# Kernel tuning notes

Hardware: AMD Instinct MI355X
Metric: run time of the kernel (lower is better)

Reference implementation:

```python
import jax, jax.numpy as jnp
import numpy as np

B, DETER, STOCH, ACT_DIM, HIDDEN, BLOCKS, DEMB = 4096, 4096, 1024, 32, 512, 8, 16
EPS = 1e-4
OUT_B = DETER // BLOCKS            # 512 per-block output
IN_B0 = 4 * HIDDEN + OUT_B          # 2560 per-block input of first hidden block-GEMM


def rmsnorm(x, g):
    return x * jax.lax.rsqrt(jnp.mean(x * x, axis=-1, keepdims=True) + EPS) * g


def setup_inputs() -> dict:
    key = jax.random.key(0)
    ks = jax.random.split(key, 16)
    n = lambda k, s: (jax.random.normal(k, s, jnp.float32) * 0.02)
    return {
        'stoch': jax.random.normal(ks[0], (B, STOCH), jnp.float32),
        'deter': jax.random.normal(ks[1], (B, DETER), jnp.float32),
        'action': jax.random.normal(ks[2], (B, ACT_DIM), jnp.float32),
        'd_emb': jax.random.normal(ks[3], (B, DEMB), jnp.float32),
        # four input branches: Linear -> RMSNorm -> SiLU
        'W0': n(ks[4], (DETER, HIDDEN)), 'b0': jnp.zeros(HIDDEN), 'g0': jnp.ones(HIDDEN),
        'W1': n(ks[5], (STOCH, HIDDEN)), 'b1': jnp.zeros(HIDDEN), 'g1': jnp.ones(HIDDEN),
        'W2': n(ks[6], (ACT_DIM, HIDDEN)), 'b2': jnp.zeros(HIDDEN), 'g2': jnp.ones(HIDDEN),
        'W3': n(ks[7], (DEMB, HIDDEN)), 'b3': jnp.zeros(HIDDEN), 'g3': jnp.ones(HIDDEN),
        # block-diagonal hidden layers (dynlayers=2)
        'Wh0': n(ks[8], (BLOCKS, IN_B0, OUT_B)), 'bh0': jnp.zeros(DETER), 'gh0': jnp.ones(DETER),
        'Wh1': n(ks[9], (BLOCKS, OUT_B, OUT_B)), 'bh1': jnp.zeros(DETER), 'gh1': jnp.ones(DETER),
        # block-diagonal GRU gate projection: deter -> 3*deter
        'Wg': n(ks[10], (BLOCKS, OUT_B, 3 * OUT_B)), 'bg': jnp.zeros(3 * DETER),
    }


def reference(stoch, deter, action, d_emb,
              W0, b0, g0, W1, b1, g1, W2, b2, g2, W3, b3, g3,
              Wh0, bh0, gh0, Wh1, bh1, gh1, Wg, bg):
    act = jax.nn.silu
    Bsz = action.shape[0]
    stoch = stoch.reshape(Bsz, -1)
    # action / clip(|action|, min=1).detach()
    action = action / jax.lax.stop_gradient(jnp.maximum(jnp.abs(action), 1.0))

    x0 = act(rmsnorm(deter @ W0 + b0, g0))
    x1 = act(rmsnorm(stoch @ W1 + b1, g1))
    x2 = act(rmsnorm(action @ W2 + b2, g2))
    x3 = act(rmsnorm(d_emb @ W3 + b3, g3))
    x = jnp.concatenate([x0, x1, x2, x3], axis=-1)          # [B, 4H]

    xg = jnp.broadcast_to(x[:, None, :], (Bsz, BLOCKS, 4 * HIDDEN))
    dg = deter.reshape(Bsz, BLOCKS, OUT_B)                   # flat2group(deter)
    h = jnp.concatenate([dg, xg], axis=-1)                   # [B, blocks, in_b0]

    # hidden layer 0: BlockLinear -> RMSNorm(full width) -> act
    h = jnp.einsum('bgi,gio->bgo', h, Wh0).reshape(Bsz, DETER) + bh0
    h = act(rmsnorm(h, gh0))
    # hidden layer 1
    h = jnp.einsum('bgi,gio->bgo', h.reshape(Bsz, BLOCKS, OUT_B), Wh1).reshape(Bsz, DETER) + bh1
    h = act(rmsnorm(h, gh1))

    # GRU gates via block-diagonal GEMM: [B, blocks, 3*out_b]
    gates = jnp.einsum('bgi,gio->bgo', h.reshape(Bsz, BLOCKS, OUT_B), Wg).reshape(Bsz, 3 * DETER) + bg
    gg = gates.reshape(Bsz, BLOCKS, 3 * OUT_B)
    reset = gg[..., :OUT_B].reshape(Bsz, DETER)
    cand = gg[..., OUT_B:2 * OUT_B].reshape(Bsz, DETER)
    update = gg[..., 2 * OUT_B:].reshape(Bsz, DETER)

    reset = jax.nn.sigmoid(reset)
    cand = jnp.tanh(reset * cand)
    update = jax.nn.sigmoid(update - 1.0)
    return update * cand + (1.0 - update) * deter
```

## Files before the change

### kernel.cpp

```cpp
#include <hip/hip_runtime.h>
#include <hip/hip_bf16.h>
#include <cstdint>

typedef __bf16 bf16x8 __attribute__((ext_vector_type(8)));
typedef float f32x4 __attribute__((ext_vector_type(4)));
typedef unsigned short u16x8 __attribute__((ext_vector_type(8)));
typedef unsigned short u16x4 __attribute__((ext_vector_type(4)));

__device__ __forceinline__ unsigned short f2bf(float f) {
  unsigned int u = __float_as_uint(f);
  u += 0x7FFFu + ((u >> 16) & 1u);
  return (unsigned short)(u >> 16);
}
__device__ __forceinline__ float bf2f(unsigned short h) {
  return __uint_as_float(((unsigned int)h) << 16);
}
__device__ __forceinline__ float frcp_(float x) { return __builtin_amdgcn_rcpf(x); }
__device__ __forceinline__ float sigmoid_fast(float x) { return frcp_(1.f + __expf(-x)); }
__device__ __forceinline__ float tanh_fast(float x) { return 1.f - 2.f * frcp_(__expf(2.f * x) + 1.f); }
__device__ __forceinline__ float siluf_(float x) { return x * sigmoid_fast(x); }

#define GLOAD_LDS16(gsrc, ldst) \
  __builtin_amdgcn_global_load_lds((const __attribute__((address_space(1))) void*)(gsrc), \
                                   (__attribute__((address_space(3))) void*)(ldst), 16, 0, 0)

#define S_BARRIER() asm volatile("s_barrier" ::: "memory")
#define LGKM0() asm volatile("s_waitcnt lgkmcnt(0)" ::: "memory")

__device__ __forceinline__ void xcd_tile(int& x, int& y, int& z) {
  const int gx = gridDim.x, gy = gridDim.y;
  const int nwg = gx * gy * gridDim.z;
  const int lin = (blockIdx.z * gy + blockIdx.y) * gx + blockIdx.x;
  const int cpx = nwg >> 3;
  const int t = (lin & 7) * cpx + (lin >> 3);
  x = t % gx;
  const int r = t / gx;
  y = r % gy;
  z = r / gy;
}

template<int F32>
__device__ __forceinline__ void gemm8_core(
    const unsigned short* __restrict__ A1, int lda1, int K1,
    const unsigned short* __restrict__ A2, int lda2, int K2,
    const unsigned short* __restrict__ Bt, int ldb,
    void* __restrict__ C, int ldc,
    int tm, int tn, unsigned short* lds)
{
  const int tid = threadIdx.x;
  const int lane = tid & 63;
  const int wave = tid >> 6;
  const int wm = (wave >> 2) * 128;
  const int wn = (wave & 3) * 64;
  const int frow = lane & 15;
  const int chunk16 = (lane >> 4) * 16;
  const int nt = (K1 + K2) >> 5;
  const int S = nt >> 1;

  auto stageA = [&](unsigned short* dstA, int ktBase) {
    const unsigned short* Ab; int alda, kloc;
    if (ktBase >= K1) { Ab = A2; alda = lda2; kloc = ktBase - K1; }
    else              { Ab = A1; alda = lda1; kloc = ktBase; }
#pragma unroll
    for (int j = 0; j < 2; ++j) {
      int o = j * 8192 + tid * 16;
      int so = o ^ (((o >> 7) & 3) << 4);
      int row = so >> 6, cb = so & 63;
      GLOAD_LDS16(Ab + (long long)(tm + row) * alda + kloc + (cb >> 1),
                  (char*)dstA + j * 8192 + wave * 1024);
    }
  };
  auto stageB = [&](unsigned short* dstB, int ktBase) {
#pragma unroll
    for (int j = 0; j < 2; ++j) {
      int o = j * 8192 + tid * 16;
      int so = o ^ (((o >> 7) & 3) << 4);
      int row = so >> 6, cb = so & 63;
      GLOAD_LDS16(Bt + (long long)(tn + row) * ldb + ktBase + (cb >> 1),
                  (char*)dstB + j * 8192 + wave * 1024);
    }
  };
  auto ldswz = [&](const unsigned short* rg, int row) -> bf16x8 {
    int o = row * 64 + chunk16;
    o ^= ((o >> 7) & 3) << 4;
    return *(const bf16x8*)((const char*)rg + o);
  };

  f32x4 acc[8][4] = {};

  stageA(lds, 0);             stageB(lds + 8192, 0);
  stageA(lds + 16384, 32);    stageB(lds + 24576, 32);
  asm volatile("s_waitcnt vmcnt(0)" ::: "memory");
  S_BARRIER();

  for (int s = 0; s < S; ++s) {
    const int t = 2 * s;
    unsigned short* b0 = lds + (t & 3) * 16384;
    unsigned short* b1 = lds + ((t + 1) & 3) * 16384;
    if (s > 0) {
      LGKM0();
      S_BARRIER();
    }
    if (s + 1 < S) {
      unsigned short* s0 = lds + ((t + 2) & 3) * 16384;
      unsigned short* s1 = lds + ((t + 3) & 3) * 16384;
      stageA(s0, (t + 2) * 32); stageB(s0 + 8192, (t + 2) * 32);
      stageA(s1, (t + 3) * 32); stageB(s1 + 8192, (t + 3) * 32);
      asm volatile("s_waitcnt vmcnt(8)" ::: "memory");
    } else {
      asm volatile("s_waitcnt vmcnt(0)" ::: "memory");
    }
    S_BARRIER();
    {
      bf16x8 av[4], bv[4];
#pragma unroll
      for (int j = 0; j < 4; ++j) bv[j] = ldswz(b0 + 8192, wn + j * 16 + frow);
#pragma unroll
      for (int i = 0; i < 4; ++i) av[i] = ldswz(b0, wm + i * 16 + frow);
      __builtin_amdgcn_s_setprio(1);
#pragma unroll
      for (int i = 0; i < 4; ++i)
#pragma unroll
        for (int j = 0; j < 4; ++j)
          acc[i][j] = __builtin_amdgcn_mfma_f32_16x16x32_bf16(av[i], bv[j], acc[i][j], 0, 0, 0);
#pragma unroll
      for (int i = 0; i < 4; ++i) av[i] = ldswz(b0, wm + 64 + i * 16 + frow);
#pragma unroll
      for (int i = 0; i < 4; ++i)
#pragma unroll
        for (int j = 0; j < 4; ++j)
          acc[4 + i][j] = __builtin_amdgcn_mfma_f32_16x16x32_bf16(av[i], bv[j], acc[4 + i][j], 0, 0, 0);
      __builtin_amdgcn_s_setprio(0);
    }
    {
      bf16x8 av[4], bv[4];
#pragma unroll
      for (int j = 0; j < 4; ++j) bv[j] = ldswz(b1 + 8192, wn + j * 16 + frow);
#pragma unroll
      for (int i = 0; i < 4; ++i) av[i] = ldswz(b1, wm + i * 16 + frow);
      __builtin_amdgcn_s_setprio(1);
#pragma unroll
      for (int i = 0; i < 4; ++i)
#pragma unroll
        for (int j = 0; j < 4; ++j)
          acc[i][j] = __builtin_amdgcn_mfma_f32_16x16x32_bf16(av[i], bv[j], acc[i][j], 0, 0, 0);
#pragma unroll
      for (int i = 0; i < 4; ++i) av[i] = ldswz(b1, wm + 64 + i * 16 + frow);
#pragma unroll
      for (int i = 0; i < 4; ++i)
#pragma unroll
        for (int j = 0; j < 4; ++j)
          acc[4 + i][j] = __builtin_amdgcn_mfma_f32_16x16x32_bf16(av[i], bv[j], acc[4 + i][j], 0, 0, 0);
      __builtin_amdgcn_s_setprio(0);
    }
  }

  const int cr = (lane >> 4) * 4;
  const int cc = lane & 15;
#pragma unroll
  for (int mf = 0; mf < 8; ++mf) {
    const int r0 = tm + wm + mf * 16 + cr;
#pragma unroll
    for (int j = 0; j < 4; ++j) {
      const int col = tn + wn + j * 16 + cc;
#pragma unroll
      for (int i = 0; i < 4; ++i) {
        if (F32) ((float*)C)[(long long)(r0 + i) * ldc + col] = acc[mf][j][i];
        else ((unsigned short*)C)[(long long)(r0 + i) * ldc + col] = f2bf(acc[mf][j][i]);
      }
    }
  }
}

__global__ __launch_bounds__(512, 2) void gemm8(
    const unsigned short* __restrict__ A1, int lda1, long long a1_bs, int K1,
    const unsigned short* __restrict__ A2, int lda2, int K2,
    const unsigned short* __restrict__ Bt, int ldb, long long bt_bs,
    unsigned short* __restrict__ C, int ldc, long long c_bs)
{
  __shared__ unsigned short lds[4 * 16384];
  int tx, ty, g;
  xcd_tile(tx, ty, g);
  gemm8_core<0>(A1 + (long long)g * a1_bs, lda1, K1, A2, lda2, K2,
                Bt + (long long)g * bt_bs, ldb,
                C + (long long)g * c_bs, ldc,
                ty * 256, tx * 256, lds);
}

struct BCfg { const unsigned short* A; int lda; int K;
              const unsigned short* Bt; int ldb; float* C; };
struct BPack { BCfg c[9]; };
__global__ __launch_bounds__(512, 2) void gemm8_branch(BPack p) {
  __shared__ unsigned short lds[4 * 16384];
  int tx, ty, z;
  xcd_tile(tx, ty, z);
  BCfg c = p.c[z];
  gemm8_core<1>(c.A, c.lda, c.K, nullptr, 0, 0, c.Bt, c.ldb, c.C, 512,
                ty * 256, tx * 256, lds);
}

__global__ __launch_bounds__(512, 2) void gemm_gru(
    const unsigned short* __restrict__ hB,
    const unsigned short* __restrict__ Wgt,
    const float* __restrict__ bg,
    const unsigned short* __restrict__ deterB,
    float* __restrict__ out)
{
  __shared__ unsigned short lds[4 * 14336];
  int txi, tyi, g;
  xcd_tile(txi, tyi, g);
  const int tm = tyi * 256;
  const int tn = txi * 192;
  const unsigned short* A  = hB + g * 512;
  const unsigned short* Bt = Wgt + (long long)g * 1536 * 512;
  const int tid = threadIdx.x, lane = tid & 63, wave = tid >> 6;
  const int wm = (wave >> 2) * 128;
  const int wv = wave & 3;
  const int frow = lane & 15, chunk16 = (lane >> 4) * 16;
  const bool wlow = (wave < 4);
  const int S = 8;

  auto stageA = [&](unsigned short* buf, int kt) {
#pragma unroll
    for (int j = 0; j < 2; ++j) {
      int o = j * 8192 + tid * 16;
      int so = o ^ (((o >> 7) & 3) << 4);
      int row = so >> 6, cb = so & 63;
      GLOAD_LDS16(A + (long long)(tm + row) * 4096 + kt + (cb >> 1),
                  (char*)buf + j * 8192 + wave * 1024);
    }
  };
  auto stageB = [&](unsigned short* buf, int kt) {
    char* bb = (char*)(buf + 8192);
    {
      int o = tid * 16;
      int so = o ^ (((o >> 7) & 3) << 4);
      int row = so >> 6, cb = so & 63;
      GLOAD_LDS16(Bt + (long long)(tn + row) * 512 + kt + (cb >> 1),
                  bb + wave * 1024);
    }
    if (tid < 256) {
      int o = 8192 + tid * 16;
      int so = o ^ (((o >> 7) & 3) << 4);
      int row = so >> 6, cb = so & 63;
      GLOAD_LDS16(Bt + (long long)(tn + row) * 512 + kt + (cb >> 1),
                  bb + 8192 + wave * 1024);
    }
  };
  auto ldA = [&](const unsigned short* buf, int row) -> bf16x8 {
    int o = row * 64 + chunk16; o ^= ((o >> 7) & 3) << 4;
    return *(const bf16x8*)((const char*)buf + o);
  };
  auto ldB = [&](const unsigned short* buf, int nf) -> bf16x8 {
    int row = wv * 48 + nf * 16 + frow;
    int o = row * 64 + chunk16; o ^= ((o >> 7) & 3) << 4;
    return *(const bf16x8*)((const char*)(buf + 8192) + o);
  };

  f32x4 acc[8][3] = {};

  stageA(lds, 0);             stageB(lds, 0);
  stageA(lds + 14336, 32);    stageB(lds + 14336, 32);
  asm volatile("s_waitcnt vmcnt(0)" ::: "memory");
  S_BARRIER();

  for (int s = 0; s < S; ++s) {
    const int t = 2 * s;
    unsigned short* b0 = lds + (t & 3) * 14336;
    unsigned short* b1 = lds + ((t + 1) & 3) * 14336;
    if (s > 0) {
      LGKM0();
      S_BARRIER();
    }
    if (s + 1 < S) {
      unsigned short* s0 = lds + ((t + 2) & 3) * 14336;
      unsigned short* s1 = lds + ((t + 3) & 3) * 14336;
      stageA(s0, (t + 2) * 32); stageB(s0, (t + 2) * 32);
      stageA(s1, (t + 3) * 32); stageB(s1, (t + 3) * 32);
      if (wlow) asm volatile("s_waitcnt vmcnt(8)" ::: "memory");
      else      asm volatile("s_waitcnt vmcnt(6)" ::: "memory");
    } else {
      asm volatile("s_waitcnt vmcnt(0)" ::: "memory");
    }
    S_BARRIER();
#pragma unroll
    for (int half = 0; half < 2; ++half) {
      const unsigned short* bb = half ? b1 : b0;
      bf16x8 av[4], bv[3];
#pragma unroll
      for (int j = 0; j < 3; ++j) bv[j] = ldB(bb, j);
#pragma unroll
      for (int i = 0; i < 4; ++i) av[i] = ldA(bb, wm + i * 16 + frow);
      __builtin_amdgcn_s_setprio(1);
#pragma unroll
      for (int i = 0; i < 4; ++i)
#pragma unroll
        for (int j = 0; j < 3; ++j)
          acc[i][j] = __builtin_amdgcn_mfma_f32_16x16x32_bf16(av[i], bv[j], acc[i][j], 0, 0, 0);
#pragma unroll
      for (int i = 0; i < 4; ++i) av[i] = ldA(bb, wm + 64 + i * 16 + frow);
#pragma unroll
      for (int i = 0; i < 4; ++i)
#pragma unroll
        for (int j = 0; j < 3; ++j)
          acc[4 + i][j] = __builtin_amdgcn_mfma_f32_16x16x32_bf16(av[i], bv[j], acc[4 + i][j], 0, 0, 0);
      __builtin_amdgcn_s_setprio(0);
    }
  }

  const int cr = (lane >> 4) * 4, cc = lane & 15;
  const int o_col = (txi * 4 + wv) * 16 + cc;
  const int gcol = g * 512 + o_col;
  const float bgr = bg[g * 1536 + o_col];
  const float bgc = bg[g * 1536 + 512 + o_col];
  const float bgu = bg[g * 1536 + 1024 + o_col];
#pragma unroll
  for (int mf = 0; mf < 8; ++mf) {
    const int r0 = tm + wm + mf * 16 + cr;
#pragma unroll
    for (int i = 0; i < 4; ++i) {
      const long long off = (long long)(r0 + i) * 4096 + gcol;
      float dt = bf2f(deterB[off]);
      float reset = sigmoid_fast(acc[mf][0][i] + bgr);
      float cand  = tanh_fast(reset * (acc[mf][1][i] + bgc));
      float upd   = sigmoid_fast(acc[mf][2][i] + bgu - 1.f);
      out[off] = upd * cand + (1.f - upd) * dt;
    }
  }
}

__device__ __forceinline__ void transpose_dev(
    const float* __restrict__ src, unsigned short* __restrict__ dst,
    int R, int C, int bx, int by, int bz, float (*t)[132])
{
  const long long bOff = (long long)bz * R * C;
  src += bOff; dst += bOff;
  const int c0 = bx * 128, r0 = by * 32;
  const int tid = threadIdx.x;
  const int tx = tid & 31, ty = tid >> 5;
#pragma unroll
  for (int j = 0; j < 4; ++j) {
    int row = ty + j * 8;
    float4 v = *(const float4*)&src[(long long)(r0 + row) * C + c0 + tx * 4];
    *(float4*)&t[row][tx * 4] = v;
  }
  __syncthreads();
#pragma unroll
  for (int j = 0; j < 4; ++j) {
    int idx = j * 256 + tid;
    int c = idx >> 3, rg = idx & 7;
    u16x4 o;
    o.x = f2bf(t[rg * 4 + 0][c]); o.y = f2bf(t[rg * 4 + 1][c]);
    o.z = f2bf(t[rg * 4 + 2][c]); o.w = f2bf(t[rg * 4 + 3][c]);
    *(u16x4*)&dst[(long long)(c0 + c) * R + r0 + rg * 4] = o;
  }
}

__device__ __forceinline__ void transpose_wg_dev(
    const float* __restrict__ src, unsigned short* __restrict__ dst,
    int bx, int by, int bz, float (*t)[132])
{
  src += (long long)bz * 512 * 1536;
  dst += (long long)bz * 1536 * 512;
  const int c0 = bx * 128, r0 = by * 32;
  const int tid = threadIdx.x;
  const int tx = tid & 31, ty = tid >> 5;
#pragma unroll
  for (int j = 0; j < 4; ++j) {
    int row = ty + j * 8;
    float4 v = *(const float4*)&src[(long long)(r0 + row) * 1536 + c0 + tx * 4];
    *(float4*)&t[row][tx * 4] = v;
  }
  __syncthreads();
#pragma unroll
  for (int j = 0; j < 4; ++j) {
    int idx = j * 256 + tid;
    int c = idx >> 3, rg = idx & 7;
    int cc = c0 + c;
    int gate = cc >> 9, o = cc & 511;
    int nn = (o >> 4) * 48 + gate * 16 + (o & 15);
    u16x4 oo;
    oo.x = f2bf(t[rg * 4 + 0][c]); oo.y = f2bf(t[rg * 4 + 1][c]);
    oo.z = f2bf(t[rg * 4 + 2][c]); oo.w = f2bf(t[rg * 4 + 3][c]);
    *(u16x4*)&dst[(long long)nn * 512 + r0 + rg * 4] = oo;
  }
}

__global__ __launch_bounds__(256) void preproc_k(
    const float* __restrict__ deter, unsigned short* __restrict__ deterB,
    const float* __restrict__ stoch, unsigned short* __restrict__ stochB,
    const float* __restrict__ W0, unsigned short* __restrict__ W0t,
    const float* __restrict__ W1, unsigned short* __restrict__ W1t,
    const float* __restrict__ Wh0, unsigned short* __restrict__ Wh0t,
    const float* __restrict__ Wh1, unsigned short* __restrict__ Wh1t,
    const float* __restrict__ Wg, unsigned short* __restrict__ Wgt)
{
  __shared__ float t[32][132];
  int b = blockIdx.x;
  if (b < 20480) {
    int i = b * 256 + threadIdx.x;
    const float* s; unsigned short* d;
    if (i < 4194304) { s = deter; d = deterB; }
    else { i -= 4194304; if (i >= 1048576) return; s = stoch; d = stochB; }
    float4 v = ((const float4*)s)[i];
    u16x4 o;
    o.x = f2bf(v.x); o.y = f2bf(v.y); o.z = f2bf(v.z); o.w = f2bf(v.w);
    ((u16x4*)d)[i] = o;
    return;
  }
  b -= 20480;
  if (b < 512)  { transpose_dev(W0, W0t, 4096, 512, b & 3, b >> 2, 0, t); return; }
  b -= 512;
  if (b < 128)  { transpose_dev(W1, W1t, 1024, 512, b & 3, b >> 2, 0, t); return; }
  b -= 128;
  if (b < 2560) { transpose_dev(Wh0, Wh0t, 2560, 512, b & 3, (b >> 2) % 80, b / 320, t); return; }
  b -= 2560;
  if (b < 512)  { transpose_dev(Wh1, Wh1t, 512, 512, b & 3, (b >> 2) & 15, b >> 6, t); return; }
  b -= 512;
  transpose_wg_dev(Wg, Wgt, b % 12, (b / 12) & 15, b / 192, t);
}

__global__ __launch_bounds__(256) void branch_epi_k(
    const float* __restrict__ yP0, const float* __restrict__ yPx,
    const float* __restrict__ yP1,
    const float* __restrict__ b0, const float* __restrict__ g0,
    const float* __restrict__ b1, const float* __restrict__ g1,
    const float* __restrict__ action, const float* __restrict__ demb,
    const float* __restrict__ W2, const float* __restrict__ b2, const float* __restrict__ g2,
    const float* __restrict__ W3, const float* __restrict__ b3, const float* __restrict__ g3,
    unsigned short* __restrict__ x)
{
  const int row = blockIdx.x, br = blockIdx.y;
  const int tid = threadIdx.x, lane = tid & 63, wave = tid >> 6;
  __shared__ float red[4];
  __shared__ float a[32];
  float v0, v1;
  const float* gg;
  if (br == 0) {
    const float* p = yP0 + (long long)row * 512;
    const float* q = yPx + (long long)row * 512;
    v0 = b0[tid]; v1 = b0[tid + 256];
#pragma unroll
    for (int c = 0; c < 4; ++c) {
      v0 += p[c * 2097152 + tid] + q[c * 2097152 + tid];
      v1 += p[c * 2097152 + tid + 256] + q[c * 2097152 + tid + 256];
    }
    gg = g0;
  } else if (br == 1) {
    const float* p = yP1 + (long long)row * 512;
    v0 = b1[tid] + p[tid];
    v1 = b1[tid + 256] + p[tid + 256];
    gg = g1;
  } else {
    const int K = (br == 3) ? 16 : 32;
    const float* W  = (br == 3) ? W3 : W2;
    const float* bb = (br == 3) ? b3 : b2;
    gg = (br == 3) ? g3 : g2;
    if (tid < K) {
      float t = (br == 3) ? demb[(long long)row * 16 + tid]
                          : action[(long long)row * 32 + tid];
      if (br == 2) t = t / fmaxf(fabsf(t), 1.f);
      a[tid] = t;
    }
    __syncthreads();
    v0 = bb[tid]; v1 = bb[tid + 256];
    for (int k = 0; k < K; ++k) {
      float av = a[k];
      v0 += av * W[k * 512 + tid];
      v1 += av * W[k * 512 + tid + 256];
    }
  }
  float ss = v0 * v0 + v1 * v1;
  for (int o = 32; o > 0; o >>= 1) ss += __shfl_xor(ss, o);
  if (lane == 0) red[wave] = ss;
  __syncthreads();
  float ms = (red[0] + red[1] + red[2] + red[3]) * (1.f / 512.f);
  float sc = rsqrtf(ms + 1e-4f);
  unsigned short* xr = x + (long long)row * 2048 + br * 512;
  xr[tid]       = f2bf(siluf_(v0 * sc * gg[tid]));
  xr[tid + 256] = f2bf(siluf_(v1 * sc * gg[tid + 256]));
}

__global__ __launch_bounds__(256) void epi_full_k(
    const unsigned short* __restrict__ y, const float* __restrict__ bias,
    const float* __restrict__ gw, unsigned short* __restrict__ h)
{
  const int row = blockIdx.x;
  __shared__ float red[4];
  const int tid = threadIdx.x, lane = tid & 63, wave = tid >> 6;
  const u16x8* yv = (const u16x8*)(y + (long long)row * 4096);
  u16x8 ta = yv[tid], tb = yv[256 + tid];
  float ba[8], bb8[8];
  *(float4*)&ba[0]  = *(const float4*)&bias[tid * 8];
  *(float4*)&ba[4]  = *(const float4*)&bias[tid * 8 + 4];
  *(float4*)&bb8[0] = *(const float4*)&bias[(256 + tid) * 8];
  *(float4*)&bb8[4] = *(const float4*)&bias[(256 + tid) * 8 + 4];
  float fa[8], fb[8];
  float ss = 0.f;
#pragma unroll
  for (int e = 0; e < 8; ++e) {
    fa[e] = bf2f(ta[e]) + ba[e];  ss += fa[e] * fa[e];
    fb[e] = bf2f(tb[e]) + bb8[e]; ss += fb[e] * fb[e];
  }
  for (int o = 32; o > 0; o >>= 1) ss += __shfl_xor(ss, o);
  if (lane == 0) red[wave] = ss;
  __syncthreads();
  float ms = (red[0] + red[1] + red[2] + red[3]) * (1.f / 4096.f);
  float sc = rsqrtf(ms + 1e-4f);
  float ga[8], gb8[8];
  *(float4*)&ga[0]  = *(const float4*)&gw[tid * 8];
  *(float4*)&ga[4]  = *(const float4*)&gw[tid * 8 + 4];
  *(float4*)&gb8[0] = *(const float4*)&gw[(256 + tid) * 8];
  *(float4*)&gb8[4] = *(const float4*)&gw[(256 + tid) * 8 + 4];
  u16x8 oa, ob;
#pragma unroll
  for (int e = 0; e < 8; ++e) {
    oa[e] = f2bf(siluf_(fa[e] * sc * ga[e]));
    ob[e] = f2bf(siluf_(fb[e] * sc * gb8[e]));
  }
  u16x8* hv = (u16x8*)(h + (long long)row * 4096);
  hv[tid] = oa;
  hv[256 + tid] = ob;
}

extern "C" void kernel_launch(void* const* d_in, const int* in_sizes, int n_in,
                              void* d_out, int out_size, void* d_ws, size_t ws_size,
                              hipStream_t stream) {
  const float* stoch  = (const float*)d_in[0];
  const float* deter  = (const float*)d_in[1];
  const float* action = (const float*)d_in[2];
  const float* demb   = (const float*)d_in[3];
  const float* W0 = (const float*)d_in[4];
  const float* b0 = (const float*)d_in[5];
  const float* g0 = (const float*)d_in[6];
  const float* W1 = (const float*)d_in[7];
  const float* b1 = (const float*)d_in[8];
  const float* g1 = (const float*)d_in[9];
  const float* W2 = (const float*)d_in[10];
  const float* b2 = (const float*)d_in[11];
  const float* g2 = (const float*)d_in[12];
  const float* W3 = (const float*)d_in[13];
  const float* b3 = (const float*)d_in[14];
  const float* g3 = (const float*)d_in[15];
  const float* Wh0 = (const float*)d_in[16];
  const float* bh0 = (const float*)d_in[17];
  const float* gh0 = (const float*)d_in[18];
  const float* Wh1 = (const float*)d_in[19];
  const float* bh1 = (const float*)d_in[20];
  const float* gh1 = (const float*)d_in[21];
  const float* Wg  = (const float*)d_in[22];
  const float* bg  = (const float*)d_in[23];
  float* out = (float*)d_out;

  char* ws = (char*)d_ws;
  unsigned short* deterB = (unsigned short*)(ws + 0);
  unsigned short* stochB = (unsigned short*)(ws + 33554432);
  unsigned short* W0t    = (unsigned short*)(ws + 41943040);
  unsigned short* W1t    = (unsigned short*)(ws + 46137344);
  unsigned short* xB     = (unsigned short*)(ws + 47185920);
  float*          yP0    = (float*)(ws + 63963136);
  unsigned short* yB     = (unsigned short*)(ws + 63963136);
  float*          yP1    = (float*)(ws + 97517568);
  unsigned short* Wh0t   = (unsigned short*)(ws + 105906176);
  unsigned short* Wgt    = (unsigned short*)(ws + 105906176);
  unsigned short* Wh1t   = (unsigned short*)(ws + 126877696);
  unsigned short* hB     = (unsigned short*)(ws + 134217728);
  float*          yPx    = (float*)(ws + 134217728);
  (void)in_sizes; (void)n_in; (void)out_size; (void)ws_size;
  Wgt = (unsigned short*)(ws + 167772160);

  dim3 b256(256);
  dim3 b512(512);
  preproc_k<<<dim3(25728), b256, 0, stream>>>(deter, deterB, stoch, stochB,
                                              W0, W0t, W1, W1t, Wh0, Wh0t,
                                              Wh1, Wh1t, Wg, Wgt);
  {
    BPack p;
    for (int z = 0; z < 8; ++z) {
      float* part = (z < 4) ? (yP0 + (long long)z * 2097152)
                            : (yPx + (long long)(z - 4) * 2097152);
      p.c[z] = { deterB + z * 512, 4096, 512, W0t + z * 512, 4096, part };
    }
    p.c[8] = { stochB, 1024, 1024, W1t, 1024, yP1 };
    gemm8_branch<<<dim3(2, 16, 9), b512, 0, stream>>>(p);
  }
  branch_epi_k<<<dim3(4096, 4), b256, 0, stream>>>(yP0, yPx, yP1, b0, g0, b1, g1,
                                                   action, demb, W2, b2, g2, W3, b3, g3, xB);
  gemm8<<<dim3(2, 16, 8), b512, 0, stream>>>(deterB, 4096, 512, 512, xB, 2048, 2048,
                                             Wh0t, 2560, 512LL * 2560, yB, 4096, 512);
  epi_full_k<<<dim3(4096), b256, 0, stream>>>(yB, bh0, gh0, hB);
  gemm8<<<dim3(2, 16, 8), b512, 0, stream>>>(hB, 4096, 512, 512, nullptr, 0, 0,
                                             Wh1t, 512, 512LL * 512, yB, 4096, 512);
  epi_full_k<<<dim3(4096), b256, 0, stream>>>(yB, bh1, gh1, hB);
  gemm_gru<<<dim3(8, 16, 8), b512, 0, stream>>>(hB, Wgt, bg, deterB, out);
}
```

Baseline: 366.9 us.

## Restructure GEMM main loops into per-tile 3-deep prefetch pipeline; store split-K partials in bf16

Both the generic block GEMM core and the GRU gate GEMM move from a two-tile-per-iteration loop with a barrier per pair to a per-K-tile loop. Each iteration prefetches the tile three steps ahead, staging A and B separately between the two MFMA halves, and uses graduated vmcnt waits so global loads overlap compute more finely. Separately, the split-K partial outputs of the deter/stoch branch GEMMs are written as bf16 instead of fp32, which roughly halves the partial-sum write and read traffic in the branch epilogue. The cost is lower precision in the summed partials and more barriers per K step.

```diff
diff --git a/kernel.cpp b/kernel.cpp
--- a/kernel.cpp
+++ b/kernel.cpp
@@ -55,7 +55,6 @@
   const int frow = lane & 15;
   const int chunk16 = (lane >> 4) * 16;
   const int nt = (K1 + K2) >> 5;
-  const int S = nt >> 1;
 
   auto stageA = [&](unsigned short* dstA, int ktBase) {
     const unsigned short* Ab; int alda, kloc;
@@ -88,71 +87,52 @@
 
   f32x4 acc[8][4] = {};
 
-  stageA(lds, 0);             stageB(lds + 8192, 0);
-  stageA(lds + 16384, 32);    stageB(lds + 24576, 32);
-  asm volatile("s_waitcnt vmcnt(0)" ::: "memory");
+#pragma unroll
+  for (int t = 0; t < 3; ++t) {
+    unsigned short* b = lds + t * 16384;
+    stageA(b, t * 32); stageB(b + 8192, t * 32);
+  }
+  asm volatile("s_waitcnt vmcnt(8)" ::: "memory");
   S_BARRIER();
 
-  for (int s = 0; s < S; ++s) {
-    const int t = 2 * s;
-    unsigned short* b0 = lds + (t & 3) * 16384;
-    unsigned short* b1 = lds + ((t + 1) & 3) * 16384;
-    if (s > 0) {
-      LGKM0();
-      S_BARRIER();
-    }
-    if (s + 1 < S) {
-      unsigned short* s0 = lds + ((t + 2) & 3) * 16384;
-      unsigned short* s1 = lds + ((t + 3) & 3) * 16384;
-      stageA(s0, (t + 2) * 32); stageB(s0 + 8192, (t + 2) * 32);
-      stageA(s1, (t + 3) * 32); stageB(s1 + 8192, (t + 3) * 32);
+  for (int T = 0; T < nt; ++T) {
+    unsigned short* b = lds + (T & 3) * 16384;
+    unsigned short* bs = lds + ((T + 3) & 3) * 16384;
+    bf16x8 av[4], bv[4];
+#pragma unroll
+    for (int j = 0; j < 4; ++j) bv[j] = ldswz(b + 8192, wn + j * 16 + frow);
+#pragma unroll
+    for (int i = 0; i < 4; ++i) av[i] = ldswz(b, wm + i * 16 + frow);
+    if (T + 3 < nt) stageA(bs, (T + 3) * 32);
+    S_BARRIER();
+    LGKM0();
+    __builtin_amdgcn_s_setprio(1);
+#pragma unroll
+    for (int i = 0; i < 4; ++i)
+#pragma unroll
+      for (int j = 0; j < 4; ++j)
+        acc[i][j] = __builtin_amdgcn_mfma_f32_16x16x32_bf16(av[i], bv[j], acc[i][j], 0, 0, 0);
+    __builtin_amdgcn_s_setprio(0);
+    bf16x8 a2[4];
+#pragma unroll
+    for (int i = 0; i < 4; ++i) a2[i] = ldswz(b, wm + 64 + i * 16 + frow);
+    if (T + 3 < nt) {
+      stageB(bs + 8192, (T + 3) * 32);
       asm volatile("s_waitcnt vmcnt(8)" ::: "memory");
-    } else {
+    } else if (T + 2 < nt) {
+      asm volatile("s_waitcnt vmcnt(4)" ::: "memory");
+    } else if (T + 1 < nt) {
       asm volatile("s_waitcnt vmcnt(0)" ::: "memory");
     }
     S_BARRIER();
-    {
-      bf16x8 av[4], bv[4];
-#pragma unroll
-      for (int j = 0; j < 4; ++j) bv[j] = ldswz(b0 + 8192, wn + j * 16 + frow);
-#pragma unroll
-      for (int i = 0; i < 4; ++i) av[i] = ldswz(b0, wm + i * 16 + frow);
-      __builtin_amdgcn_s_setprio(1);
-#pragma unroll
-      for (int i = 0; i < 4; ++i)
-#pragma unroll
-        for (int j = 0; j < 4; ++j)
-          acc[i][j] = __builtin_amdgcn_mfma_f32_16x16x32_bf16(av[i], bv[j], acc[i][j], 0, 0, 0);
-#pragma unroll
-      for (int i = 0; i < 4; ++i) av[i] = ldswz(b0, wm + 64 + i * 16 + frow);
-#pragma unroll
-      for (int i = 0; i < 4; ++i)
-#pragma unroll
-        for (int j = 0; j < 4; ++j)
-          acc[4 + i][j] = __builtin_amdgcn_mfma_f32_16x16x32_bf16(av[i], bv[j], acc[4 + i][j], 0, 0, 0);
-      __builtin_amdgcn_s_setprio(0);
-    }
-    {
-      bf16x8 av[4], bv[4];
-#pragma unroll
-      for (int j = 0; j < 4; ++j) bv[j] = ldswz(b1 + 8192, wn + j * 16 + frow);
-#pragma unroll
-      for (int i = 0; i < 4; ++i) av[i] = ldswz(b1, wm + i * 16 + frow);
-      __builtin_amdgcn_s_setprio(1);
-#pragma unroll
-      for (int i = 0; i < 4; ++i)
-#pragma unroll
-        for (int j = 0; j < 4; ++j)
-          acc[i][j] = __builtin_amdgcn_mfma_f32_16x16x32_bf16(av[i], bv[j], acc[i][j], 0, 0, 0);
-#pragma unroll
-      for (int i = 0; i < 4; ++i) av[i] = ldswz(b1, wm + 64 + i * 16 + frow);
-#pragma unroll
-      for (int i = 0; i < 4; ++i)
-#pragma unroll
-        for (int j = 0; j < 4; ++j)
-          acc[4 + i][j] = __builtin_amdgcn_mfma_f32_16x16x32_bf16(av[i], bv[j], acc[4 + i][j], 0, 0, 0);
-      __builtin_amdgcn_s_setprio(0);
-    }
+    LGKM0();
+    __builtin_amdgcn_s_setprio(1);
+#pragma unroll
+    for (int i = 0; i < 4; ++i)
+#pragma unroll
+      for (int j = 0; j < 4; ++j)
+        acc[4 + i][j] = __builtin_amdgcn_mfma_f32_16x16x32_bf16(a2[i], bv[j], acc[4 + i][j], 0, 0, 0);
+    __builtin_amdgcn_s_setprio(0);
   }
 
   const int cr = (lane >> 4) * 4;
@@ -188,14 +168,14 @@
 }
 
 struct BCfg { const unsigned short* A; int lda; int K;
-              const unsigned short* Bt; int ldb; float* C; };
+              const unsigned short* Bt; int ldb; unsigned short* C; };
 struct BPack { BCfg c[9]; };
 __global__ __launch_bounds__(512, 2) void gemm8_branch(BPack p) {
   __shared__ unsigned short lds[4 * 16384];
   int tx, ty, z;
   xcd_tile(tx, ty, z);
   BCfg c = p.c[z];
-  gemm8_core<1>(c.A, c.lda, c.K, nullptr, 0, 0, c.Bt, c.ldb, c.C, 512,
+  gemm8_core<0>(c.A, c.lda, c.K, nullptr, 0, 0, c.Bt, c.ldb, c.C, 512,
                 ty * 256, tx * 256, lds);
 }
 
@@ -218,7 +198,7 @@
   const int wv = wave & 3;
   const int frow = lane & 15, chunk16 = (lane >> 4) * 16;
   const bool wlow = (wave < 4);
-  const int S = 8;
+  const int nt = 16;
 
   auto stageA = [&](unsigned short* buf, int kt) {
 #pragma unroll
@@ -256,56 +236,66 @@
     int o = row * 64 + chunk16; o ^= ((o >> 7) & 3) << 4;
     return *(const bf16x8*)((const char*)(buf + 8192) + o);
   };
+  auto vm_gate = [&](int n_lo, int n_hi) {
+    if (wlow) {
+      if (n_lo == 8) asm volatile("s_waitcnt vmcnt(8)" ::: "memory");
+      else if (n_lo == 4) asm volatile("s_waitcnt vmcnt(4)" ::: "memory");
+      else asm volatile("s_waitcnt vmcnt(0)" ::: "memory");
+    } else {
+      if (n_hi == 6) asm volatile("s_waitcnt vmcnt(6)" ::: "memory");
+      else if (n_hi == 3) asm volatile("s_waitcnt vmcnt(3)" ::: "memory");
+      else asm volatile("s_waitcnt vmcnt(0)" ::: "memory");
+    }
+  };
 
   f32x4 acc[8][3] = {};
 
-  stageA(lds, 0);             stageB(lds, 0);
-  stageA(lds + 14336, 32);    stageB(lds + 14336, 32);
-  asm volatile("s_waitcnt vmcnt(0)" ::: "memory");
+#pragma unroll
+  for (int t = 0; t < 3; ++t) {
+    unsigned short* b = lds + t * 14336;
+    stageA(b, t * 32); stageB(b, t * 32);
+  }
+  vm_gate(8, 6);
   S_BARRIER();
 
-  for (int s = 0; s < S; ++s) {
-    const int t = 2 * s;
-    unsigned short* b0 = lds + (t & 3) * 14336;
-    unsigned short* b1 = lds + ((t + 1) & 3) * 14336;
-    if (s > 0) {
-      LGKM0();
-      S_BARRIER();
-    }
-    if (s + 1 < S) {
-      unsigned short* s0 = lds + ((t + 2) & 3) * 14336;
-      unsigned short* s1 = lds + ((t + 3) & 3) * 14336;
-      stageA(s0, (t + 2) * 32); stageB(s0, (t + 2) * 32);
-      stageA(s1, (t + 3) * 32); stageB(s1, (t + 3) * 32);
-      if (wlow) asm volatile("s_waitcnt vmcnt(8)" ::: "memory");
-      else      asm volatile("s_waitcnt vmcnt(6)" ::: "memory");
-    } else {
-      asm volatile("s_waitcnt vmcnt(0)" ::: "memory");
-    }
+  for (int T = 0; T < nt; ++T) {
+    unsigned short* b = lds + (T & 3) * 14336;
+    unsigned short* bs = lds + ((T + 3) & 3) * 14336;
+    bf16x8 av[4], bv[3];
+#pragma unroll
+    for (int j = 0; j < 3; ++j) bv[j] = ldB(b, j);
+#pragma unroll
+    for (int i = 0; i < 4; ++i) av[i] = ldA(b, wm + i * 16 + frow);
+    if (T + 3 < nt) stageA(bs, (T + 3) * 32);
     S_BARRIER();
-#pragma unroll
-    for (int half = 0; half < 2; ++half) {
-      const unsigned short* bb = half ? b1 : b0;
-      bf16x8 av[4], bv[3];
-#pragma unroll
-      for (int j = 0; j < 3; ++j) bv[j] = ldB(bb, j);
-#pragma unroll
-      for (int i = 0; i < 4; ++i) av[i] = ldA(bb, wm + i * 16 + frow);
-      __builtin_amdgcn_s_setprio(1);
-#pragma unroll
-      for (int i = 0; i < 4; ++i)
-#pragma unroll
-        for (int j = 0; j < 3; ++j)
-          acc[i][j] = __builtin_amdgcn_mfma_f32_16x16x32_bf16(av[i], bv[j], acc[i][j], 0, 0, 0);
-#pragma unroll
-      for (int i = 0; i < 4; ++i) av[i] = ldA(bb, wm + 64 + i * 16 + frow);
-#pragma unroll
-      for (int i = 0; i < 4; ++i)
-#pragma unroll
-        for (int j = 0; j < 3; ++j)
-          acc[4 + i][j] = __builtin_amdgcn_mfma_f32_16x16x32_bf16(av[i], bv[j], acc[4 + i][j], 0, 0, 0);
-      __builtin_amdgcn_s_setprio(0);
-    }
+    LGKM0();
+    __builtin_amdgcn_s_setprio(1);
+#pragma unroll
+    for (int i = 0; i < 4; ++i)
+#pragma unroll
+      for (int j = 0; j < 3; ++j)
+        acc[i][j] = __builtin_amdgcn_mfma_f32_16x16x32_bf16(av[i], bv[j], acc[i][j], 0, 0, 0);
+    __builtin_amdgcn_s_setprio(0);
+    bf16x8 a2[4];
+#pragma unroll
+    for (int i = 0; i < 4; ++i) a2[i] = ldA(b, wm + 64 + i * 16 + frow);
+    if (T + 3 < nt) {
+      stageB(bs, (T + 3) * 32);
+      vm_gate(8, 6);
+    } else if (T + 2 < nt) {
+      vm_gate(4, 3);
+    } else if (T + 1 < nt) {
+      vm_gate(0, 0);
+    }
+    S_BARRIER();
+    LGKM0();
+    __builtin_amdgcn_s_setprio(1);
+#pragma unroll
+    for (int i = 0; i < 4; ++i)
+#pragma unroll
+      for (int j = 0; j < 3; ++j)
+        acc[4 + i][j] = __builtin_amdgcn_mfma_f32_16x16x32_bf16(a2[i], bv[j], acc[4 + i][j], 0, 0, 0);
+    __builtin_amdgcn_s_setprio(0);
   }
 
   const int cr = (lane >> 4) * 4, cc = lane & 15;
@@ -421,8 +411,7 @@
 }
 
 __global__ __launch_bounds__(256) void branch_epi_k(
-    const float* __restrict__ yP0, const float* __restrict__ yPx,
-    const float* __restrict__ yP1,
+    const unsigned short* __restrict__ yP0b, const unsigned short* __restrict__ yP1b,
     const float* __restrict__ b0, const float* __restrict__ g0,
     const float* __restrict__ b1, const float* __restrict__ g1,
     const float* __restrict__ action, const float* __restrict__ demb,
@@ -437,19 +426,18 @@
   float v0, v1;
   const float* gg;
   if (br == 0) {
-    const float* p = yP0 + (long long)row * 512;
-    const float* q = yPx + (long long)row * 512;
+    const unsigned short* p = yP0b + (long long)row * 512;
     v0 = b0[tid]; v1 = b0[tid + 256];
 #pragma unroll
-    for (int c = 0; c < 4; ++c) {
-      v0 += p[c * 2097152 + tid] + q[c * 2097152 + tid];
-      v1 += p[c * 2097152 + tid + 256] + q[c * 2097152 + tid + 256];
+    for (int c = 0; c < 8; ++c) {
+      v0 += bf2f(p[(long long)c * 2097152 + tid]);
+      v1 += bf2f(p[(long long)c * 2097152 + tid + 256]);
     }
     gg = g0;
   } else if (br == 1) {
-    const float* p = yP1 + (long long)row * 512;
-    v0 = b1[tid] + p[tid];
-    v1 = b1[tid + 256] + p[tid + 256];
+    const unsigned short* p = yP1b + (long long)row * 512;
+    v0 = b1[tid] + bf2f(p[tid]);
+    v1 = b1[tid + 256] + bf2f(p[tid + 256]);
     gg = g1;
   } else {
     const int K = (br == 3) ? 16 : 32;
@@ -558,16 +546,14 @@
   unsigned short* W0t    = (unsigned short*)(ws + 41943040);
   unsigned short* W1t    = (unsigned short*)(ws + 46137344);
   unsigned short* xB     = (unsigned short*)(ws + 47185920);
-  float*          yP0    = (float*)(ws + 63963136);
+  unsigned short* yP0b   = (unsigned short*)(ws + 63963136);
   unsigned short* yB     = (unsigned short*)(ws + 63963136);
-  float*          yP1    = (float*)(ws + 97517568);
+  unsigned short* yP1b   = (unsigned short*)(ws + 97517568);
   unsigned short* Wh0t   = (unsigned short*)(ws + 105906176);
-  unsigned short* Wgt    = (unsigned short*)(ws + 105906176);
   unsigned short* Wh1t   = (unsigned short*)(ws + 126877696);
   unsigned short* hB     = (unsigned short*)(ws + 134217728);
-  float*          yPx    = (float*)(ws + 134217728);
+  unsigned short* Wgt    = (unsigned short*)(ws + 167772160);
   (void)in_sizes; (void)n_in; (void)out_size; (void)ws_size;
-  Wgt = (unsigned short*)(ws + 167772160);
 
   dim3 b256(256);
   dim3 b512(512);
@@ -576,15 +562,13 @@
                                               Wh1, Wh1t, Wg, Wgt);
   {
     BPack p;
-    for (int z = 0; z < 8; ++z) {
-      float* part = (z < 4) ? (yP0 + (long long)z * 2097152)
-                            : (yPx + (long long)(z - 4) * 2097152);
-      p.c[z] = { deterB + z * 512, 4096, 512, W0t + z * 512, 4096, part };
-    }
-    p.c[8] = { stochB, 1024, 1024, W1t, 1024, yP1 };
+    for (int z = 0; z < 8; ++z)
+      p.c[z] = { deterB + z * 512, 4096, 512, W0t + z * 512, 4096,
+                 yP0b + (long long)z * 2097152 };
+    p.c[8] = { stochB, 1024, 1024, W1t, 1024, yP1b };
     gemm8_branch<<<dim3(2, 16, 9), b512, 0, stream>>>(p);
   }
-  branch_epi_k<<<dim3(4096, 4), b256, 0, stream>>>(yP0, yPx, yP1, b0, g0, b1, g1,
+  branch_epi_k<<<dim3(4096, 4), b256, 0, stream>>>(yP0b, yP1b, b0, g0, b1, g1,
                                                    action, demb, W2, b2, g2, W3, b3, g3, xB);
   gemm8<<<dim3(2, 16, 8), b512, 0, stream>>>(deterB, 4096, 512, 512, xB, 2048, 2048,
                                              Wh0t, 2560, 512LL * 2560, yB, 4096, 512);
```

Measured after the change: 327.4 us. 1.12x faster.
